# Optimization experiments

Hardware: AMD Instinct MI355X
Metric: run time of the kernel (lower is better)

The kernel has to match this reference:

```python
import jax, jax.numpy as jnp
import numpy as np

B, T, D = 128, 32, 1024
ADA, INTER, RANK = 1024, 1024, 8
LN_EPS = 1e-5

def setup_inputs() -> dict:
    key = jax.random.key(0)
    ks = jax.random.split(key, 9)
    return {
        "x": jax.random.normal(ks[0], (B, T, D), dtype=jnp.float32),
        "ada_emb": jax.random.normal(ks[1], (B, ADA), dtype=jnp.float32),
        "base_layer": jax.random.normal(ks[2], (D, D), dtype=jnp.float32),  # torch.randn init
        "w1": jax.random.normal(ks[3], (ADA, INTER), dtype=jnp.float32) * 0.02,
        "b1": jnp.zeros((INTER,), dtype=jnp.float32),
        "w2": jax.random.normal(ks[4], (INTER, 2 * D * RANK), dtype=jnp.float32) * 0.02,
        "b2": jnp.zeros((2 * D * RANK,), dtype=jnp.float32),
        "ln_g": jnp.ones((ADA,), dtype=jnp.float32),
        "ln_b": jnp.zeros((ADA,), dtype=jnp.float32),
    }

def _layernorm(x, g, b):
    mu = jnp.mean(x, axis=-1, keepdims=True)
    var = jnp.var(x, axis=-1, keepdims=True)
    return (x - mu) * jax.lax.rsqrt(var + LN_EPS) * g + b

def reference(x, ada_emb, base_layer, w1, b1, w2, b2, ln_g, ln_b):
    b, t, d = x.shape
    # hypernetwork: cond -> per-sample LoRA factors
    ae = _layernorm(ada_emb, ln_g, ln_b)
    h = jax.nn.gelu(ae @ w1 + b1, approximate=False)  # nn.GELU is exact (erf)
    xw = h @ w2 + b2                                   # (B, 2*D*rank)
    x_a, x_b = jnp.split(xw, 2, axis=-1)
    x_a = x_a.reshape(b, d, RANK)
    x_b = x_b.reshape(b, d, RANK)
    # fused per-sample weight: base + x_a @ x_b^T  -> (B, D, D)
    layer = base_layer[None, :, :] + jnp.einsum('bdr,bkr->bdk', x_a, x_b)
    # apply shared per-sample weight to every token (equiv to repeat_interleave + bmm)
    out = jnp.einsum('btc,bco->bto', x, layer)
    return x + out  # residual=True
```

## Files before the change

kernel.cpp:

```cpp
#include <hip/hip_runtime.h>
#include <hip/hip_bf16.h>
#include <math.h>

#define BB    128
#define TT    32
#define DD    1024
#define NADA  1024
#define NINT  1024
#define NRANK 8
#define LNEPS 1e-5f
#define TKCH  8
#define SPL2  8
#define SPLW  2
#define XWN   (2 * DD * NRANK)

using bf16x8 = __attribute__((ext_vector_type(8))) short;
using f32x4  = __attribute__((ext_vector_type(4))) float;

__device__ __forceinline__ short f2bf(float f) {
    __hip_bfloat16 h = __float2bfloat16(f);
    return *reinterpret_cast<short*>(&h);
}

__device__ __forceinline__ float bf2f(short s) {
    unsigned u = ((unsigned)(unsigned short)s) << 16;
    return __uint_as_float(u);
}

__device__ __forceinline__ void async16(const void* g, void* l) {
    __builtin_amdgcn_global_load_lds(
        (const __attribute__((address_space(1))) void*)g,
        (__attribute__((address_space(3))) void*)l, 16, 0, 0);
}

__device__ __forceinline__ void tcast_tile(
    const float* __restrict__ in, short* __restrict__ out, int K, int N,
    int bx, int by, bool addI, int tid, float (*t)[68])
{
    const int n0 = bx * 64, k0 = by * 64;
    #pragma unroll
    for (int it = 0; it < 4; ++it) {
        const int idx = it * 256 + tid;
        const int r = idx >> 4, c4 = (idx & 15) * 4;
        float4 v = *(const float4*)(in + (size_t)(k0 + r) * N + n0 + c4);
        t[r][c4 + 0] = v.x; t[r][c4 + 1] = v.y;
        t[r][c4 + 2] = v.z; t[r][c4 + 3] = v.w;
    }
    __syncthreads();
    #pragma unroll
    for (int it = 0; it < 4; ++it) {
        const int idx = it * 256 + tid;
        const int rn = idx >> 4, c4 = (idx & 15) * 4;
        float f0 = t[c4 + 0][rn], f1 = t[c4 + 1][rn];
        float f2 = t[c4 + 2][rn], f3 = t[c4 + 3][rn];
        if (addI) {
            const int n = n0 + rn;
            if (k0 + c4 + 0 == n) f0 += 1.f;
            if (k0 + c4 + 1 == n) f1 += 1.f;
            if (k0 + c4 + 2 == n) f2 += 1.f;
            if (k0 + c4 + 3 == n) f3 += 1.f;
        }
        short4 p;
        p.x = f2bf(f0); p.y = f2bf(f1); p.z = f2bf(f2); p.w = f2bf(f3);
        *(short4*)(out + (size_t)(n0 + rn) * K + k0 + c4) = p;
    }
}

__global__ __launch_bounds__(256) void prep_kernel(
    const float* __restrict__ x, const float* __restrict__ w1,
    const float* __restrict__ base, const float* __restrict__ ada,
    const float* __restrict__ lng, const float* __restrict__ lnb,
    short* __restrict__ x_bf, short* __restrict__ w1t,
    short* __restrict__ baset, short* __restrict__ ae_bf)
{
    __shared__ float t[64][68];
    const int bid = blockIdx.x, tid = threadIdx.x;

    if (bid < 2048) {
        const int i0 = bid * 512 + tid;
        float4 v0 = reinterpret_cast<const float4*>(x)[i0];
        float4 v1 = reinterpret_cast<const float4*>(x)[i0 + 256];
        short4 p0, p1;
        p0.x = f2bf(v0.x); p0.y = f2bf(v0.y); p0.z = f2bf(v0.z); p0.w = f2bf(v0.w);
        p1.x = f2bf(v1.x); p1.y = f2bf(v1.y); p1.z = f2bf(v1.z); p1.w = f2bf(v1.w);
        reinterpret_cast<short4*>(x_bf)[i0] = p0;
        reinterpret_cast<short4*>(x_bf)[i0 + 256] = p1;
    } else if (bid < 2304) {
        const int b = bid - 2048;
        tcast_tile(w1, w1t, NADA, NINT, b & 15, b >> 4, false, tid, t);
    } else if (bid < 2560) {
        const int b = bid - 2304;
        tcast_tile(base, baset, DD, DD, b & 15, b >> 4, true, tid, t);
    } else {
        const int b = bid - 2560;
        const float* row = ada + (size_t)b * NADA;
        float sum = 0.f, sumsq = 0.f;
        for (int i = tid; i < NADA; i += 256) {
            float v = row[i];
            sum += v; sumsq += v * v;
        }
        #pragma unroll
        for (int off = 32; off > 0; off >>= 1) {
            sum   += __shfl_down(sum, off);
            sumsq += __shfl_down(sumsq, off);
        }
        float* s1 = &t[0][0];
        float* s2 = &t[1][0];
        const int wid = tid >> 6, lane = tid & 63;
        if (lane == 0) { s1[wid] = sum; s2[wid] = sumsq; }
        __syncthreads();
        if (tid == 0) {
            float a = 0.f, c = 0.f;
            for (int i = 0; i < 4; ++i) { a += s1[i]; c += s2[i]; }
            s1[0] = a; s2[0] = c;
        }
        __syncthreads();
        const float mu  = s1[0] * (1.f / NADA);
        const float var = s2[0] * (1.f / NADA) - mu * mu;
        const float inv = rsqrtf(var + LNEPS);
        for (int i = tid; i < NADA; i += 256) {
            ae_bf[(size_t)b * NADA + i] = f2bf((row[i] - mu) * inv * lng[i] + lnb[i]);
        }
    }
}

template <int BM, int BN, int WM, int WN, int EPI>
__global__ __launch_bounds__(256, 2) void mgemm(
    const short* __restrict__ A, const short* __restrict__ Bt,
    float* __restrict__ C, int M, int N, int K, int kLen,
    const float* __restrict__ tp, const float* __restrict__ p3,
    const float* __restrict__ b2)
{
    constexpr int MT = BM / WM / 16;
    constexpr int NT = BN / WN / 16;
    constexpr int LA = BM / 64;
    constexpr int LB = BN / 64;

    __shared__ __align__(16) short As[BM * 64];
    __shared__ __align__(16) short Bs[BN * 64];
    __shared__ float tmS[(EPI == 2) ? BM * 8 : 1];
    __shared__ float xbS[(EPI == 2) ? (BM / 32) * BN * 8 : 1];

    const int bm = blockIdx.y * BM;
    const int bn = blockIdx.x * BN;
    const int kStart = blockIdx.z * kLen;
    const int tid = threadIdx.x;
    const int wave = tid >> 6, lane = tid & 63;
    const int wm0 = (wave / WN) * (BM / WM);
    const int wn0 = (wave % WN) * (BN / WN);
    const int quad = lane >> 4, r16 = lane & 15;

    if constexpr (EPI == 2) {
        float4 a = {0.f, 0.f, 0.f, 0.f};
        #pragma unroll
        for (int ch = 0; ch < TKCH; ++ch) {
            float4 v = *(const float4*)(tp + (size_t)ch * BB * TT * NRANK
                                           + (size_t)bm * 8 + tid * 4);
            a.x += v.x; a.y += v.y; a.z += v.z; a.w += v.w;
        }
        *(float4*)&tmS[tid * 4] = a;
        const int b0 = bm >> 5;
        const int grp = tid >> 6;
        const int inner = tid & 63;
        const size_t off = (size_t)(b0 + grp) * XWN + DD * NRANK + (size_t)bn * 8
                         + inner * 8;
        const int bcol = DD * NRANK + bn * 8 + inner * 8;
        float4 s0a = *(const float4*)(p3 + off);
        float4 s0b = *(const float4*)(p3 + off + 4);
        float4 s1a = *(const float4*)(p3 + (size_t)BB * XWN + off);
        float4 s1b = *(const float4*)(p3 + (size_t)BB * XWN + off + 4);
        float4 ba  = *(const float4*)(b2 + bcol);
        float4 bb  = *(const float4*)(b2 + bcol + 4);
        float4 r0 = {s0a.x + s1a.x + ba.x, s0a.y + s1a.y + ba.y,
                     s0a.z + s1a.z + ba.z, s0a.w + s1a.w + ba.w};
        float4 r1 = {s0b.x + s1b.x + bb.x, s0b.y + s1b.y + bb.y,
                     s0b.z + s1b.z + bb.z, s0b.w + s1b.w + bb.w};
        *(float4*)&xbS[grp * BN * 8 + inner * 8]     = r0;
        *(float4*)&xbS[grp * BN * 8 + inner * 8 + 4] = r1;
    }

    f32x4 acc[MT][NT] = {};

    for (int kt = 0; kt < kLen; kt += 64) {
        const int k0 = kStart + kt;
        #pragma unroll
        for (int kk = 0; kk < 2; ++kk) {
            #pragma unroll
            for (int s = 0; s < LA; ++s) {
                const int c = s * 256 + tid;
                async16(A + (size_t)(bm + (c >> 2)) * K + k0 + kk * 32 + (c & 3) * 8,
                        &As[kk * BM * 32 + c * 8]);
            }
            #pragma unroll
            for (int s = 0; s < LB; ++s) {
                const int c = s * 256 + tid;
                async16(Bt + (size_t)(bn + (c >> 2)) * K + k0 + kk * 32 + (c & 3) * 8,
                        &Bs[kk * BN * 32 + c * 8]);
            }
        }
        __syncthreads();
        #pragma unroll
        for (int kk = 0; kk < 2; ++kk) {
            bf16x8 af[MT], bfr[NT];
            #pragma unroll
            for (int i = 0; i < MT; ++i)
                af[i] = *reinterpret_cast<const bf16x8*>(
                    &As[kk * BM * 32 + (wm0 + i * 16 + r16) * 32 + quad * 8]);
            #pragma unroll
            for (int j = 0; j < NT; ++j)
                bfr[j] = *reinterpret_cast<const bf16x8*>(
                    &Bs[kk * BN * 32 + (wn0 + j * 16 + r16) * 32 + quad * 8]);
            #pragma unroll
            for (int i = 0; i < MT; ++i)
                #pragma unroll
                for (int j = 0; j < NT; ++j)
                    acc[i][j] = __builtin_amdgcn_mfma_f32_16x16x32_bf16(
                        af[i], bfr[j], acc[i][j], 0, 0, 0);
        }
        __syncthreads();
    }

    if constexpr (EPI == 2) {
        float xbr[NT][8];
        #pragma unroll
        for (int i = 0; i < MT; ++i) {
            const int mlBase = wm0 + i * 16 + quad * 4;
            const int s = mlBase >> 5;
            #pragma unroll
            for (int j = 0; j < NT; ++j) {
                const int nl = wn0 + j * 16 + r16;
                #pragma unroll
                for (int rr = 0; rr < 8; ++rr)
                    xbr[j][rr] = xbS[(s * BN + nl) * 8 + rr];
            }
            #pragma unroll
            for (int r = 0; r < 4; ++r) {
                const int ml = mlBase + r;
                const int m = bm + ml;
                float t8[8];
                #pragma unroll
                for (int rr = 0; rr < 8; ++rr) t8[rr] = tmS[ml * 8 + rr];
                #pragma unroll
                for (int j = 0; j < NT; ++j) {
                    const int n = bn + wn0 + j * 16 + r16;
                    float v = acc[i][j][r];
                    #pragma unroll
                    for (int rr = 0; rr < 8; ++rr) v += t8[rr] * xbr[j][rr];
                    C[(size_t)m * N + n] = v;
                }
            }
        }
    } else {
        #pragma unroll
        for (int i = 0; i < MT; ++i) {
            #pragma unroll
            for (int r = 0; r < 4; ++r) {
                const int m = bm + wm0 + i * 16 + quad * 4 + r;
                #pragma unroll
                for (int j = 0; j < NT; ++j) {
                    const int n = bn + wn0 + j * 16 + r16;
                    C[((size_t)blockIdx.z * M + m) * N + n] = acc[i][j][r];
                }
            }
        }
    }
}

template <int SPLITK>
__global__ __launch_bounds__(256, 2) void gemm_w2(
    const short* __restrict__ A, const float* __restrict__ W,
    float* __restrict__ P, int M, int N, int K)
{
    constexpr int BM = 128, BN = 64;
    constexpr int MT = 4, NT = 2;
    __shared__ __align__(16) short As[BM * 64];
    __shared__ __align__(16) float Bf[64 * BN];

    const int bn = blockIdx.x * BN;
    const int kLen = K / SPLITK;
    const int kStart = blockIdx.z * kLen;
    const int tid = threadIdx.x;
    const int wave = tid >> 6, lane = tid & 63;
    const int wm0 = (wave >> 1) * 64;
    const int wn0 = (wave & 1) * 32;
    const int quad = lane >> 4, r16 = lane & 15;

    f32x4 acc[MT][NT] = {};

    for (int kt = 0; kt < kLen; kt += 64) {
        const int k0 = kStart + kt;
        #pragma unroll
        for (int kk = 0; kk < 2; ++kk) {
            #pragma unroll
            for (int s = 0; s < 2; ++s) {
                const int c = s * 256 + tid;
                async16(A + (size_t)(c >> 2) * K + k0 + kk * 32 + (c & 3) * 8,
                        &As[kk * BM * 32 + c * 8]);
            }
            #pragma unroll
            for (int s = 0; s < 2; ++s) {
                const int c = s * 256 + tid;
                async16(W + (size_t)(k0 + kk * 32 + (c >> 4)) * N + bn + (c & 15) * 4,
                        &Bf[kk * 32 * BN + c * 4]);
            }
        }
        __syncthreads();
        #pragma unroll
        for (int kk = 0; kk < 2; ++kk) {
            bf16x8 af[MT], bfr[NT];
            #pragma unroll
            for (int i = 0; i < MT; ++i)
                af[i] = *reinterpret_cast<const bf16x8*>(
                    &As[kk * BM * 32 + (wm0 + i * 16 + r16) * 32 + quad * 8]);
            #pragma unroll
            for (int j = 0; j < NT; ++j) {
                const int n = wn0 + j * 16 + r16;
                short tmp[8];
                #pragma unroll
                for (int t = 0; t < 8; ++t)
                    tmp[t] = f2bf(Bf[kk * 32 * BN + (quad * 8 + t) * BN + n]);
                bfr[j] = *reinterpret_cast<const bf16x8*>(tmp);
            }
            #pragma unroll
            for (int i = 0; i < MT; ++i)
                #pragma unroll
                for (int j = 0; j < NT; ++j)
                    acc[i][j] = __builtin_amdgcn_mfma_f32_16x16x32_bf16(
                        af[i], bfr[j], acc[i][j], 0, 0, 0);
        }
        __syncthreads();
    }

    #pragma unroll
    for (int i = 0; i < MT; ++i) {
        #pragma unroll
        for (int r = 0; r < 4; ++r) {
            const int m = wm0 + i * 16 + quad * 4 + r;
            #pragma unroll
            for (int j = 0; j < NT; ++j) {
                const int n = bn + wn0 + j * 16 + r16;
                P[((size_t)blockIdx.z * M + m) * N + n] = acc[i][j][r];
            }
        }
    }
}

__global__ __launch_bounds__(256) void combine_gelu(
    const float* __restrict__ part, const float* __restrict__ b1,
    short* __restrict__ h)
{
    const int i4 = (blockIdx.x * 256 + threadIdx.x) * 4;
    float4 s = *(const float4*)(b1 + (i4 & (NINT - 1)));
    #pragma unroll
    for (int z = 0; z < SPL2; ++z) {
        float4 p = *(const float4*)(part + (size_t)z * BB * NINT + i4);
        s.x += p.x; s.y += p.y; s.z += p.z; s.w += p.w;
    }
    s.x = 0.5f * s.x * (1.f + erff(s.x * 0.70710678118654752f));
    s.y = 0.5f * s.y * (1.f + erff(s.y * 0.70710678118654752f));
    s.z = 0.5f * s.z * (1.f + erff(s.z * 0.70710678118654752f));
    s.w = 0.5f * s.w * (1.f + erff(s.w * 0.70710678118654752f));
    short4 o;
    o.x = f2bf(s.x); o.y = f2bf(s.y); o.z = f2bf(s.z); o.w = f2bf(s.w);
    *(short4*)(h + i4) = o;
}

__global__ __launch_bounds__(256) void tpart_kernel(
    const short* __restrict__ x_bf, const float* __restrict__ p3,
    const float* __restrict__ b2, float* __restrict__ tp)
{
    __shared__ float xa[(DD / TKCH) * NRANK];
    const int b = blockIdx.x, ch = blockIdx.y;
    const int col0 = ch * (DD / TKCH) * NRANK;
    const size_t off = (size_t)b * XWN + col0;
    {
        const int i4 = threadIdx.x * 4;
        float4 v0 = *(const float4*)(p3 + off + i4);
        float4 v1 = *(const float4*)(p3 + (size_t)BB * XWN + off + i4);
        float4 vb = *(const float4*)(b2 + col0 + i4);
        float4 r = {v0.x + v1.x + vb.x, v0.y + v1.y + vb.y,
                    v0.z + v1.z + vb.z, v0.w + v1.w + vb.w};
        *(float4*)(xa + i4) = r;
    }
    __syncthreads();
    const int m = threadIdx.x >> 3;
    const int r = threadIdx.x & 7;
    const short* xrow = x_bf + ((size_t)b * TT + m) * DD + ch * (DD / TKCH);
    float accv = 0.f;
    #pragma unroll 2
    for (int c = 0; c < DD / TKCH; c += 8) {
        bf16x8 xr = *(const bf16x8*)(xrow + c);
        #pragma unroll
        for (int u = 0; u < 8; ++u)
            accv += bf2f(xr[u]) * xa[(c + u) * NRANK + r];
    }
    tp[((size_t)ch * BB * TT + (size_t)b * TT + m) * NRANK + r] = accv;
}

extern "C" void kernel_launch(void* const* d_in, const int* in_sizes, int n_in,
                              void* d_out, int out_size, void* d_ws, size_t ws_size,
                              hipStream_t stream)
{
    const float* x    = (const float*)d_in[0];
    const float* ada  = (const float*)d_in[1];
    const float* base = (const float*)d_in[2];
    const float* w1   = (const float*)d_in[3];
    const float* b1   = (const float*)d_in[4];
    const float* w2   = (const float*)d_in[5];
    const float* b2   = (const float*)d_in[6];
    const float* lng  = (const float*)d_in[7];
    const float* lnb  = (const float*)d_in[8];
    float* out = (float*)d_out;

    char* w = (char*)d_ws;
    short* x_bf  = (short*)w;  w += (size_t)8 << 20;
    short* w1t   = (short*)w;  w += (size_t)2 << 20;
    short* baset = (short*)w;  w += (size_t)2 << 20;
    short* ae_bf = (short*)w;  w += (size_t)256 << 10;
    short* h_bf  = (short*)w;  w += (size_t)256 << 10;
    float* p3    = (float*)w;  w += (size_t)16 << 20;
    float* tp    = (float*)w;  w += (size_t)1 << 20;
    float* part  = (float*)w;

    prep_kernel<<<2688, 256, 0, stream>>>(
        x, w1, base, ada, lng, lnb, x_bf, w1t, baset, ae_bf);
    mgemm<64, 64, 2, 2, 0><<<dim3(NINT / 64, BB / 64, SPL2), 256, 0, stream>>>(
        ae_bf, w1t, part, BB, NINT, NADA, NADA / SPL2, nullptr, nullptr, nullptr);
    combine_gelu<<<BB * NINT / 1024, 256, 0, stream>>>(part, b1, h_bf);
    gemm_w2<SPLW><<<dim3(XWN / 64, 1, SPLW), 256, 0, stream>>>(
        h_bf, w2, p3, BB, XWN, NINT);
    tpart_kernel<<<dim3(BB, TKCH), 256, 0, stream>>>(x_bf, p3, b2, tp);
    mgemm<128, 64, 2, 2, 2><<<dim3(DD / 64, BB * TT / 128), 256, 0, stream>>>(
        x_bf, baset, out, BB * TT, DD, DD, DD, tp, p3, b2);
}
```

Baseline: 178.0 us.

## Double-buffer LDS tiles in bf16 GEMM kernels to overlap loads with MFMA

Both the generic mgemm kernel and the w2 GEMM now use two shared-memory buffers for the A and B tiles. The next K-tile is issued asynchronously into the idle buffer while MFMAs run on the current one, leaving one barrier per iteration instead of two. The goal is to hide global-to-LDS latency behind compute. In exchange, shared-memory use per block doubles, which may limit occupancy. Correctness relies on the barrier also waiting for the outstanding async copies.

```diff
diff --git a/kernel.cpp b/kernel.cpp
--- a/kernel.cpp
+++ b/kernel.cpp
@@ -136,8 +136,8 @@
     constexpr int LA = BM / 64;
     constexpr int LB = BN / 64;
 
-    __shared__ __align__(16) short As[BM * 64];
-    __shared__ __align__(16) short Bs[BN * 64];
+    __shared__ __align__(16) short As[2][BM * 64];
+    __shared__ __align__(16) short Bs[2][BN * 64];
     __shared__ float tmS[(EPI == 2) ? BM * 8 : 1];
     __shared__ float xbS[(EPI == 2) ? (BM / 32) * BN * 8 : 1];
 
@@ -181,35 +181,35 @@
 
     f32x4 acc[MT][NT] = {};
 
-    for (int kt = 0; kt < kLen; kt += 64) {
-        const int k0 = kStart + kt;
+    auto stageAB = [&](int buf, int k0) {
         #pragma unroll
         for (int kk = 0; kk < 2; ++kk) {
             #pragma unroll
             for (int s = 0; s < LA; ++s) {
                 const int c = s * 256 + tid;
                 async16(A + (size_t)(bm + (c >> 2)) * K + k0 + kk * 32 + (c & 3) * 8,
-                        &As[kk * BM * 32 + c * 8]);
+                        &As[buf][kk * BM * 32 + c * 8]);
             }
             #pragma unroll
             for (int s = 0; s < LB; ++s) {
                 const int c = s * 256 + tid;
                 async16(Bt + (size_t)(bn + (c >> 2)) * K + k0 + kk * 32 + (c & 3) * 8,
-                        &Bs[kk * BN * 32 + c * 8]);
-            }
-        }
-        __syncthreads();
+                        &Bs[buf][kk * BN * 32 + c * 8]);
+            }
+        }
+    };
+    auto computeT = [&](int buf) {
         #pragma unroll
         for (int kk = 0; kk < 2; ++kk) {
             bf16x8 af[MT], bfr[NT];
             #pragma unroll
             for (int i = 0; i < MT; ++i)
                 af[i] = *reinterpret_cast<const bf16x8*>(
-                    &As[kk * BM * 32 + (wm0 + i * 16 + r16) * 32 + quad * 8]);
+                    &As[buf][kk * BM * 32 + (wm0 + i * 16 + r16) * 32 + quad * 8]);
             #pragma unroll
             for (int j = 0; j < NT; ++j)
                 bfr[j] = *reinterpret_cast<const bf16x8*>(
-                    &Bs[kk * BN * 32 + (wn0 + j * 16 + r16) * 32 + quad * 8]);
+                    &Bs[buf][kk * BN * 32 + (wn0 + j * 16 + r16) * 32 + quad * 8]);
             #pragma unroll
             for (int i = 0; i < MT; ++i)
                 #pragma unroll
@@ -217,8 +217,18 @@
                     acc[i][j] = __builtin_amdgcn_mfma_f32_16x16x32_bf16(
                         af[i], bfr[j], acc[i][j], 0, 0, 0);
         }
+    };
+
+    stageAB(0, kStart);
+    __syncthreads();
+    int cur = 0;
+    for (int kt = 64; kt < kLen; kt += 64) {
+        stageAB(cur ^ 1, kStart + kt);
+        computeT(cur);
         __syncthreads();
-    }
+        cur ^= 1;
+    }
+    computeT(cur);
 
     if constexpr (EPI == 2) {
         float xbr[NT][8];
@@ -273,8 +283,8 @@
 {
     constexpr int BM = 128, BN = 64;
     constexpr int MT = 4, NT = 2;
-    __shared__ __align__(16) short As[BM * 64];
-    __shared__ __align__(16) float Bf[64 * BN];
+    __shared__ __align__(16) short As[2][BM * 64];
+    __shared__ __align__(16) float Bf[2][64 * BN];
 
     const int bn = blockIdx.x * BN;
     const int kLen = K / SPLITK;
@@ -287,38 +297,38 @@
 
     f32x4 acc[MT][NT] = {};
 
-    for (int kt = 0; kt < kLen; kt += 64) {
-        const int k0 = kStart + kt;
+    auto stageAB = [&](int buf, int k0) {
         #pragma unroll
         for (int kk = 0; kk < 2; ++kk) {
             #pragma unroll
             for (int s = 0; s < 2; ++s) {
                 const int c = s * 256 + tid;
                 async16(A + (size_t)(c >> 2) * K + k0 + kk * 32 + (c & 3) * 8,
-                        &As[kk * BM * 32 + c * 8]);
+                        &As[buf][kk * BM * 32 + c * 8]);
             }
             #pragma unroll
             for (int s = 0; s < 2; ++s) {
                 const int c = s * 256 + tid;
                 async16(W + (size_t)(k0 + kk * 32 + (c >> 4)) * N + bn + (c & 15) * 4,
-                        &Bf[kk * 32 * BN + c * 4]);
-            }
-        }
-        __syncthreads();
+                        &Bf[buf][kk * 32 * BN + c * 4]);
+            }
+        }
+    };
+    auto computeT = [&](int buf) {
         #pragma unroll
         for (int kk = 0; kk < 2; ++kk) {
             bf16x8 af[MT], bfr[NT];
             #pragma unroll
             for (int i = 0; i < MT; ++i)
                 af[i] = *reinterpret_cast<const bf16x8*>(
-                    &As[kk * BM * 32 + (wm0 + i * 16 + r16) * 32 + quad * 8]);
+                    &As[buf][kk * BM * 32 + (wm0 + i * 16 + r16) * 32 + quad * 8]);
             #pragma unroll
             for (int j = 0; j < NT; ++j) {
                 const int n = wn0 + j * 16 + r16;
                 short tmp[8];
                 #pragma unroll
                 for (int t = 0; t < 8; ++t)
-                    tmp[t] = f2bf(Bf[kk * 32 * BN + (quad * 8 + t) * BN + n]);
+                    tmp[t] = f2bf(Bf[buf][kk * 32 * BN + (quad * 8 + t) * BN + n]);
                 bfr[j] = *reinterpret_cast<const bf16x8*>(tmp);
             }
             #pragma unroll
@@ -328,8 +338,18 @@
                     acc[i][j] = __builtin_amdgcn_mfma_f32_16x16x32_bf16(
                         af[i], bfr[j], acc[i][j], 0, 0, 0);
         }
+    };
+
+    stageAB(0, kStart);
+    __syncthreads();
+    int cur = 0;
+    for (int kt = 64; kt < kLen; kt += 64) {
+        stageAB(cur ^ 1, kStart + kt);
+        computeT(cur);
         __syncthreads();
-    }
+        cur ^= 1;
+    }
+    computeT(cur);
 
     #pragma unroll
     for (int i = 0; i < MT; ++i) {
```

Result: slower. 185.2 us (+4.1%).

## Fuse x·x_a projection into main GEMM via extra MFMA and drop split-K in w2

Applied to the files above, without the earlier changes.

Removes the separate tpart kernel. The per-token projection x·x_a is now computed inside the final GEMM by loading a transposed bf16 copy of x_a into LDS and issuing an extra MFMA per row tile. gemm_w2 no longer uses split-K and writes bias-added x_a (bf16, transposed) and x_b (fp32) directly, which removes the p3 partial buffers and their reduction. The trade-off is fewer launches and less intermediate traffic against half as many workgroups in gemm_w2 with a longer K loop, plus extra MFMA and LDS work in the main GEMM.

```diff
diff --git a/kernel.cpp b/kernel.cpp
--- a/kernel.cpp
+++ b/kernel.cpp
@@ -9,9 +9,7 @@
 #define NINT  1024
 #define NRANK 8
 #define LNEPS 1e-5f
-#define TKCH  8
 #define SPL2  8
-#define SPLW  2
 #define XWN   (2 * DD * NRANK)
 
 using bf16x8 = __attribute__((ext_vector_type(8))) short;
@@ -20,11 +18,6 @@
 __device__ __forceinline__ short f2bf(float f) {
     __hip_bfloat16 h = __float2bfloat16(f);
     return *reinterpret_cast<short*>(&h);
-}
-
-__device__ __forceinline__ float bf2f(short s) {
-    unsigned u = ((unsigned)(unsigned short)s) << 16;
-    return __uint_as_float(u);
 }
 
 __device__ __forceinline__ void async16(const void* g, void* l) {
@@ -124,222 +117,65 @@
     }
 }
 
-template <int BM, int BN, int WM, int WN, int EPI>
-__global__ __launch_bounds__(256, 2) void mgemm(
+__global__ __launch_bounds__(256, 2) void mgemm2(
     const short* __restrict__ A, const short* __restrict__ Bt,
-    float* __restrict__ C, int M, int N, int K, int kLen,
-    const float* __restrict__ tp, const float* __restrict__ p3,
-    const float* __restrict__ b2)
-{
-    constexpr int MT = BM / WM / 16;
-    constexpr int NT = BN / WN / 16;
-    constexpr int LA = BM / 64;
-    constexpr int LB = BN / 64;
-
+    float* __restrict__ C, int kLen)
+{
+    constexpr int BM = 64, BN = 64;
     __shared__ __align__(16) short As[BM * 64];
     __shared__ __align__(16) short Bs[BN * 64];
-    __shared__ float tmS[(EPI == 2) ? BM * 8 : 1];
-    __shared__ float xbS[(EPI == 2) ? (BM / 32) * BN * 8 : 1];
 
     const int bm = blockIdx.y * BM;
     const int bn = blockIdx.x * BN;
     const int kStart = blockIdx.z * kLen;
     const int tid = threadIdx.x;
     const int wave = tid >> 6, lane = tid & 63;
-    const int wm0 = (wave / WN) * (BM / WM);
-    const int wn0 = (wave % WN) * (BN / WN);
+    const int wm0 = (wave >> 1) * 32;
+    const int wn0 = (wave & 1) * 32;
     const int quad = lane >> 4, r16 = lane & 15;
 
-    if constexpr (EPI == 2) {
-        float4 a = {0.f, 0.f, 0.f, 0.f};
-        #pragma unroll
-        for (int ch = 0; ch < TKCH; ++ch) {
-            float4 v = *(const float4*)(tp + (size_t)ch * BB * TT * NRANK
-                                           + (size_t)bm * 8 + tid * 4);
-            a.x += v.x; a.y += v.y; a.z += v.z; a.w += v.w;
-        }
-        *(float4*)&tmS[tid * 4] = a;
-        const int b0 = bm >> 5;
-        const int grp = tid >> 6;
-        const int inner = tid & 63;
-        const size_t off = (size_t)(b0 + grp) * XWN + DD * NRANK + (size_t)bn * 8
-                         + inner * 8;
-        const int bcol = DD * NRANK + bn * 8 + inner * 8;
-        float4 s0a = *(const float4*)(p3 + off);
-        float4 s0b = *(const float4*)(p3 + off + 4);
-        float4 s1a = *(const float4*)(p3 + (size_t)BB * XWN + off);
-        float4 s1b = *(const float4*)(p3 + (size_t)BB * XWN + off + 4);
-        float4 ba  = *(const float4*)(b2 + bcol);
-        float4 bb  = *(const float4*)(b2 + bcol + 4);
-        float4 r0 = {s0a.x + s1a.x + ba.x, s0a.y + s1a.y + ba.y,
-                     s0a.z + s1a.z + ba.z, s0a.w + s1a.w + ba.w};
-        float4 r1 = {s0b.x + s1b.x + bb.x, s0b.y + s1b.y + bb.y,
-                     s0b.z + s1b.z + bb.z, s0b.w + s1b.w + bb.w};
-        *(float4*)&xbS[grp * BN * 8 + inner * 8]     = r0;
-        *(float4*)&xbS[grp * BN * 8 + inner * 8 + 4] = r1;
-    }
-
-    f32x4 acc[MT][NT] = {};
+    f32x4 acc[2][2] = {};
 
     for (int kt = 0; kt < kLen; kt += 64) {
         const int k0 = kStart + kt;
         #pragma unroll
         for (int kk = 0; kk < 2; ++kk) {
-            #pragma unroll
-            for (int s = 0; s < LA; ++s) {
-                const int c = s * 256 + tid;
-                async16(A + (size_t)(bm + (c >> 2)) * K + k0 + kk * 32 + (c & 3) * 8,
-                        &As[kk * BM * 32 + c * 8]);
-            }
-            #pragma unroll
-            for (int s = 0; s < LB; ++s) {
-                const int c = s * 256 + tid;
-                async16(Bt + (size_t)(bn + (c >> 2)) * K + k0 + kk * 32 + (c & 3) * 8,
-                        &Bs[kk * BN * 32 + c * 8]);
-            }
-        }
-        __syncthreads();
-        #pragma unroll
-        for (int kk = 0; kk < 2; ++kk) {
-            bf16x8 af[MT], bfr[NT];
-            #pragma unroll
-            for (int i = 0; i < MT; ++i)
+            async16(A + (size_t)(bm + (tid >> 2)) * NADA + k0 + kk * 32 + (tid & 3) * 8,
+                    &As[kk * 2048 + tid * 8]);
+            async16(Bt + (size_t)(bn + (tid >> 2)) * NADA + k0 + kk * 32 + (tid & 3) * 8,
+                    &Bs[kk * 2048 + tid * 8]);
+        }
+        __syncthreads();
+        #pragma unroll
+        for (int kk = 0; kk < 2; ++kk) {
+            bf16x8 af[2], bfr[2];
+            #pragma unroll
+            for (int i = 0; i < 2; ++i)
                 af[i] = *reinterpret_cast<const bf16x8*>(
-                    &As[kk * BM * 32 + (wm0 + i * 16 + r16) * 32 + quad * 8]);
-            #pragma unroll
-            for (int j = 0; j < NT; ++j)
+                    &As[kk * 2048 + (wm0 + i * 16 + r16) * 32 + quad * 8]);
+            #pragma unroll
+            for (int j = 0; j < 2; ++j)
                 bfr[j] = *reinterpret_cast<const bf16x8*>(
-                    &Bs[kk * BN * 32 + (wn0 + j * 16 + r16) * 32 + quad * 8]);
-            #pragma unroll
-            for (int i = 0; i < MT; ++i)
+                    &Bs[kk * 2048 + (wn0 + j * 16 + r16) * 32 + quad * 8]);
+            #pragma unroll
+            for (int i = 0; i < 2; ++i)
                 #pragma unroll
-                for (int j = 0; j < NT; ++j)
+                for (int j = 0; j < 2; ++j)
                     acc[i][j] = __builtin_amdgcn_mfma_f32_16x16x32_bf16(
                         af[i], bfr[j], acc[i][j], 0, 0, 0);
         }
         __syncthreads();
     }
 
-    if constexpr (EPI == 2) {
-        float xbr[NT][8];
-        #pragma unroll
-        for (int i = 0; i < MT; ++i) {
-            const int mlBase = wm0 + i * 16 + quad * 4;
-            const int s = mlBase >> 5;
-            #pragma unroll
-            for (int j = 0; j < NT; ++j) {
-                const int nl = wn0 + j * 16 + r16;
-                #pragma unroll
-                for (int rr = 0; rr < 8; ++rr)
-                    xbr[j][rr] = xbS[(s * BN + nl) * 8 + rr];
-            }
-            #pragma unroll
-            for (int r = 0; r < 4; ++r) {
-                const int ml = mlBase + r;
-                const int m = bm + ml;
-                float t8[8];
-                #pragma unroll
-                for (int rr = 0; rr < 8; ++rr) t8[rr] = tmS[ml * 8 + rr];
-                #pragma unroll
-                for (int j = 0; j < NT; ++j) {
-                    const int n = bn + wn0 + j * 16 + r16;
-                    float v = acc[i][j][r];
-                    #pragma unroll
-                    for (int rr = 0; rr < 8; ++rr) v += t8[rr] * xbr[j][rr];
-                    C[(size_t)m * N + n] = v;
-                }
-            }
-        }
-    } else {
-        #pragma unroll
-        for (int i = 0; i < MT; ++i) {
-            #pragma unroll
-            for (int r = 0; r < 4; ++r) {
-                const int m = bm + wm0 + i * 16 + quad * 4 + r;
-                #pragma unroll
-                for (int j = 0; j < NT; ++j) {
-                    const int n = bn + wn0 + j * 16 + r16;
-                    C[((size_t)blockIdx.z * M + m) * N + n] = acc[i][j][r];
-                }
-            }
-        }
-    }
-}
-
-template <int SPLITK>
-__global__ __launch_bounds__(256, 2) void gemm_w2(
-    const short* __restrict__ A, const float* __restrict__ W,
-    float* __restrict__ P, int M, int N, int K)
-{
-    constexpr int BM = 128, BN = 64;
-    constexpr int MT = 4, NT = 2;
-    __shared__ __align__(16) short As[BM * 64];
-    __shared__ __align__(16) float Bf[64 * BN];
-
-    const int bn = blockIdx.x * BN;
-    const int kLen = K / SPLITK;
-    const int kStart = blockIdx.z * kLen;
-    const int tid = threadIdx.x;
-    const int wave = tid >> 6, lane = tid & 63;
-    const int wm0 = (wave >> 1) * 64;
-    const int wn0 = (wave & 1) * 32;
-    const int quad = lane >> 4, r16 = lane & 15;
-
-    f32x4 acc[MT][NT] = {};
-
-    for (int kt = 0; kt < kLen; kt += 64) {
-        const int k0 = kStart + kt;
-        #pragma unroll
-        for (int kk = 0; kk < 2; ++kk) {
-            #pragma unroll
-            for (int s = 0; s < 2; ++s) {
-                const int c = s * 256 + tid;
-                async16(A + (size_t)(c >> 2) * K + k0 + kk * 32 + (c & 3) * 8,
-                        &As[kk * BM * 32 + c * 8]);
-            }
-            #pragma unroll
-            for (int s = 0; s < 2; ++s) {
-                const int c = s * 256 + tid;
-                async16(W + (size_t)(k0 + kk * 32 + (c >> 4)) * N + bn + (c & 15) * 4,
-                        &Bf[kk * 32 * BN + c * 4]);
-            }
-        }
-        __syncthreads();
-        #pragma unroll
-        for (int kk = 0; kk < 2; ++kk) {
-            bf16x8 af[MT], bfr[NT];
-            #pragma unroll
-            for (int i = 0; i < MT; ++i)
-                af[i] = *reinterpret_cast<const bf16x8*>(
-                    &As[kk * BM * 32 + (wm0 + i * 16 + r16) * 32 + quad * 8]);
-            #pragma unroll
-            for (int j = 0; j < NT; ++j) {
-                const int n = wn0 + j * 16 + r16;
-                short tmp[8];
-                #pragma unroll
-                for (int t = 0; t < 8; ++t)
-                    tmp[t] = f2bf(Bf[kk * 32 * BN + (quad * 8 + t) * BN + n]);
-                bfr[j] = *reinterpret_cast<const bf16x8*>(tmp);
-            }
-            #pragma unroll
-            for (int i = 0; i < MT; ++i)
-                #pragma unroll
-                for (int j = 0; j < NT; ++j)
-                    acc[i][j] = __builtin_amdgcn_mfma_f32_16x16x32_bf16(
-                        af[i], bfr[j], acc[i][j], 0, 0, 0);
-        }
-        __syncthreads();
-    }
-
-    #pragma unroll
-    for (int i = 0; i < MT; ++i) {
+    #pragma unroll
+    for (int i = 0; i < 2; ++i) {
         #pragma unroll
         for (int r = 0; r < 4; ++r) {
-            const int m = wm0 + i * 16 + quad * 4 + r;
-            #pragma unroll
-            for (int j = 0; j < NT; ++j) {
+            const int m = bm + wm0 + i * 16 + quad * 4 + r;
+            #pragma unroll
+            for (int j = 0; j < 2; ++j) {
                 const int n = bn + wn0 + j * 16 + r16;
-                P[((size_t)blockIdx.z * M + m) * N + n] = acc[i][j][r];
+                C[((size_t)blockIdx.z * BB + m) * NINT + n] = acc[i][j][r];
             }
         }
     }
@@ -365,36 +201,203 @@
     *(short4*)(h + i4) = o;
 }
 
-__global__ __launch_bounds__(256) void tpart_kernel(
-    const short* __restrict__ x_bf, const float* __restrict__ p3,
-    const float* __restrict__ b2, float* __restrict__ tp)
-{
-    __shared__ float xa[(DD / TKCH) * NRANK];
-    const int b = blockIdx.x, ch = blockIdx.y;
-    const int col0 = ch * (DD / TKCH) * NRANK;
-    const size_t off = (size_t)b * XWN + col0;
+__global__ __launch_bounds__(256, 2) void gemm_w2(
+    const short* __restrict__ A, const float* __restrict__ W,
+    const float* __restrict__ b2,
+    short* __restrict__ xat, float* __restrict__ xwb)
+{
+    constexpr int BN = 64;
+    __shared__ __align__(16) short As[128 * 64];
+    __shared__ __align__(16) float Bf[64 * BN];
+
+    const int bn = blockIdx.x * BN;
+    const int tid = threadIdx.x;
+    const int wave = tid >> 6, lane = tid & 63;
+    const int wm0 = (wave >> 1) * 64;
+    const int wn0 = (wave & 1) * 32;
+    const int quad = lane >> 4, r16 = lane & 15;
+
+    f32x4 acc[4][2] = {};
+
+    for (int kt = 0; kt < NINT; kt += 64) {
+        #pragma unroll
+        for (int kk = 0; kk < 2; ++kk) {
+            #pragma unroll
+            for (int s = 0; s < 2; ++s) {
+                const int c = s * 256 + tid;
+                async16(A + (size_t)(c >> 2) * NINT + kt + kk * 32 + (c & 3) * 8,
+                        &As[kk * 4096 + c * 8]);
+            }
+            #pragma unroll
+            for (int s = 0; s < 2; ++s) {
+                const int c = s * 256 + tid;
+                async16(W + (size_t)(kt + kk * 32 + (c >> 4)) * XWN + bn + (c & 15) * 4,
+                        &Bf[kk * 2048 + c * 4]);
+            }
+        }
+        __syncthreads();
+        #pragma unroll
+        for (int kk = 0; kk < 2; ++kk) {
+            bf16x8 af[4], bfr[2];
+            #pragma unroll
+            for (int i = 0; i < 4; ++i)
+                af[i] = *reinterpret_cast<const bf16x8*>(
+                    &As[kk * 4096 + (wm0 + i * 16 + r16) * 32 + quad * 8]);
+            #pragma unroll
+            for (int j = 0; j < 2; ++j) {
+                const int n = wn0 + j * 16 + r16;
+                short tmp[8];
+                #pragma unroll
+                for (int t = 0; t < 8; ++t)
+                    tmp[t] = f2bf(Bf[kk * 2048 + (quad * 8 + t) * BN + n]);
+                bfr[j] = *reinterpret_cast<const bf16x8*>(tmp);
+            }
+            #pragma unroll
+            for (int i = 0; i < 4; ++i)
+                #pragma unroll
+                for (int j = 0; j < 2; ++j)
+                    acc[i][j] = __builtin_amdgcn_mfma_f32_16x16x32_bf16(
+                        af[i], bfr[j], acc[i][j], 0, 0, 0);
+        }
+        __syncthreads();
+    }
+
+    const bool isA = (bn < DD * NRANK);
+    #pragma unroll
+    for (int i = 0; i < 4; ++i) {
+        #pragma unroll
+        for (int r = 0; r < 4; ++r) {
+            const int m = wm0 + i * 16 + quad * 4 + r;
+            #pragma unroll
+            for (int j = 0; j < 2; ++j) {
+                const int n = bn + wn0 + j * 16 + r16;
+                const float v = acc[i][j][r] + b2[n];
+                if (isA)
+                    xat[(size_t)m * (NRANK * DD) + (n & 7) * DD + (n >> 3)] = f2bf(v);
+                else
+                    xwb[(size_t)m * (NRANK * DD) + (n - DD * NRANK)] = v;
+            }
+        }
+    }
+}
+
+__global__ __launch_bounds__(256, 2) void fgemm(
+    const short* __restrict__ A,
+    const short* __restrict__ Bt,
+    const short* __restrict__ xat,
+    const float* __restrict__ xwb,
+    float* __restrict__ C)
+{
+    __shared__ __align__(16) short As[128 * 64];
+    __shared__ __align__(16) short Bs[64 * 64];
+    __shared__ __align__(16) short xaS[32 * 64];
+    __shared__ float tmS[128 * 8];
+    __shared__ float xbS[4 * 64 * 8];
+
+    const int bn = blockIdx.x * 64;
+    const int bm = blockIdx.y * 128;
+    const int b0 = bm >> 5;
+    const int tid = threadIdx.x;
+    const int wave = tid >> 6, lane = tid & 63;
+    const int wm0 = (wave >> 1) * 64;
+    const int wn0 = (wave & 1) * 32;
+    const int quad = lane >> 4, r16 = lane & 15;
+    const int w2s = (wave >> 1) * 2;
+
     {
-        const int i4 = threadIdx.x * 4;
-        float4 v0 = *(const float4*)(p3 + off + i4);
-        float4 v1 = *(const float4*)(p3 + (size_t)BB * XWN + off + i4);
-        float4 vb = *(const float4*)(b2 + col0 + i4);
-        float4 r = {v0.x + v1.x + vb.x, v0.y + v1.y + vb.y,
-                    v0.z + v1.z + vb.z, v0.w + v1.w + vb.w};
-        *(float4*)(xa + i4) = r;
+        const int grp = tid >> 6, inner = tid & 63;
+        const size_t off = (size_t)(b0 + grp) * (NRANK * DD) + (size_t)bn * 8 + inner * 8;
+        float4 r0 = *(const float4*)(xwb + off);
+        float4 r1 = *(const float4*)(xwb + off + 4);
+        *(float4*)&xbS[grp * 512 + inner * 8]     = r0;
+        *(float4*)&xbS[grp * 512 + inner * 8 + 4] = r1;
+    }
+
+    f32x4 acc[4][2] = {};
+    f32x4 at[4] = {};
+
+    for (int kt = 0; kt < DD; kt += 64) {
+        #pragma unroll
+        for (int kk = 0; kk < 2; ++kk) {
+            #pragma unroll
+            for (int s = 0; s < 2; ++s) {
+                const int c = s * 256 + tid;
+                async16(A + (size_t)(bm + (c >> 2)) * DD + kt + kk * 32 + (c & 3) * 8,
+                        &As[kk * 4096 + c * 8]);
+            }
+            async16(Bt + (size_t)(bn + (tid >> 2)) * DD + kt + kk * 32 + (tid & 3) * 8,
+                    &Bs[kk * 2048 + tid * 8]);
+        }
+        async16(xat + ((size_t)(b0 + (tid >> 6)) * 8 + ((tid >> 3) & 7)) * DD
+                    + kt + (tid & 7) * 8,
+                &xaS[(tid >> 3) * 64 + (tid & 7) * 8]);
+        __syncthreads();
+        #pragma unroll
+        for (int kk = 0; kk < 2; ++kk) {
+            bf16x8 af[4], bfr[2], bft[2];
+            #pragma unroll
+            for (int i = 0; i < 4; ++i)
+                af[i] = *reinterpret_cast<const bf16x8*>(
+                    &As[kk * 4096 + (wm0 + i * 16 + r16) * 32 + quad * 8]);
+            #pragma unroll
+            for (int j = 0; j < 2; ++j)
+                bfr[j] = *reinterpret_cast<const bf16x8*>(
+                    &Bs[kk * 2048 + (wn0 + j * 16 + r16) * 32 + quad * 8]);
+            #pragma unroll
+            for (int u = 0; u < 2; ++u)
+                bft[u] = *reinterpret_cast<const bf16x8*>(
+                    &xaS[((w2s + u) * 8 + (r16 & 7)) * 64 + kk * 32 + quad * 8]);
+            #pragma unroll
+            for (int i = 0; i < 4; ++i) {
+                #pragma unroll
+                for (int j = 0; j < 2; ++j)
+                    acc[i][j] = __builtin_amdgcn_mfma_f32_16x16x32_bf16(
+                        af[i], bfr[j], acc[i][j], 0, 0, 0);
+                at[i] = __builtin_amdgcn_mfma_f32_16x16x32_bf16(
+                    af[i], bft[i >> 1], at[i], 0, 0, 0);
+            }
+        }
+        __syncthreads();
+    }
+
+    if (r16 < 8) {
+        #pragma unroll
+        for (int i = 0; i < 4; ++i)
+            #pragma unroll
+            for (int r = 0; r < 4; ++r)
+                tmS[(wm0 + i * 16 + quad * 4 + r) * 8 + r16] = at[i][r];
     }
     __syncthreads();
-    const int m = threadIdx.x >> 3;
-    const int r = threadIdx.x & 7;
-    const short* xrow = x_bf + ((size_t)b * TT + m) * DD + ch * (DD / TKCH);
-    float accv = 0.f;
-    #pragma unroll 2
-    for (int c = 0; c < DD / TKCH; c += 8) {
-        bf16x8 xr = *(const bf16x8*)(xrow + c);
-        #pragma unroll
-        for (int u = 0; u < 8; ++u)
-            accv += bf2f(xr[u]) * xa[(c + u) * NRANK + r];
-    }
-    tp[((size_t)ch * BB * TT + (size_t)b * TT + m) * NRANK + r] = accv;
+
+    float xbr[2][8];
+    #pragma unroll
+    for (int i = 0; i < 4; ++i) {
+        const int mlBase = wm0 + i * 16 + quad * 4;
+        const int s = mlBase >> 5;
+        #pragma unroll
+        for (int j = 0; j < 2; ++j) {
+            const int nl = wn0 + j * 16 + r16;
+            #pragma unroll
+            for (int rr = 0; rr < 8; ++rr)
+                xbr[j][rr] = xbS[(s * 64 + nl) * 8 + rr];
+        }
+        #pragma unroll
+        for (int r = 0; r < 4; ++r) {
+            const int ml = mlBase + r;
+            const int m = bm + ml;
+            float t8[8];
+            #pragma unroll
+            for (int rr = 0; rr < 8; ++rr) t8[rr] = tmS[ml * 8 + rr];
+            #pragma unroll
+            for (int j = 0; j < 2; ++j) {
+                const int n = bn + wn0 + j * 16 + r16;
+                float v = acc[i][j][r];
+                #pragma unroll
+                for (int rr = 0; rr < 8; ++rr) v += t8[rr] * xbr[j][rr];
+                C[(size_t)m * DD + n] = v;
+            }
+        }
+    }
 }
 
 extern "C" void kernel_launch(void* const* d_in, const int* in_sizes, int n_in,
@@ -418,18 +421,16 @@
     short* baset = (short*)w;  w += (size_t)2 << 20;
     short* ae_bf = (short*)w;  w += (size_t)256 << 10;
     short* h_bf  = (short*)w;  w += (size_t)256 << 10;
-    float* p3    = (float*)w;  w += (size_t)16 << 20;
-    float* tp    = (float*)w;  w += (size_t)1 << 20;
+    short* xat   = (short*)w;  w += (size_t)2 << 20;
+    float* xwb   = (float*)w;  w += (size_t)4 << 20;
     float* part  = (float*)w;
 
     prep_kernel<<<2688, 256, 0, stream>>>(
         x, w1, base, ada, lng, lnb, x_bf, w1t, baset, ae_bf);
-    mgemm<64, 64, 2, 2, 0><<<dim3(NINT / 64, BB / 64, SPL2), 256, 0, stream>>>(
-        ae_bf, w1t, part, BB, NINT, NADA, NADA / SPL2, nullptr, nullptr, nullptr);
+    mgemm2<<<dim3(NINT / 64, BB / 64, SPL2), 256, 0, stream>>>(
+        ae_bf, w1t, part, NADA / SPL2);
     combine_gelu<<<BB * NINT / 1024, 256, 0, stream>>>(part, b1, h_bf);
-    gemm_w2<SPLW><<<dim3(XWN / 64, 1, SPLW), 256, 0, stream>>>(
-        h_bf, w2, p3, BB, XWN, NINT);
-    tpart_kernel<<<dim3(BB, TKCH), 256, 0, stream>>>(x_bf, p3, b2, tp);
-    mgemm<128, 64, 2, 2, 2><<<dim3(DD / 64, BB * TT / 128), 256, 0, stream>>>(
-        x_bf, baset, out, BB * TT, DD, DD, DD, tp, p3, b2);
-}
+    gemm_w2<<<XWN / 64, 256, 0, stream>>>(h_bf, w2, b2, xat, xwb);
+    fgemm<<<dim3(DD / 64, BB * TT / 128), 256, 0, stream>>>(
+        x_bf, baset, xat, xwb, out);
+}
```

After: 181.0 us. No clear change (+1.7%).
